# Kernel tuning notes

Hardware: AMD Instinct MI355X
Metric: run time of the kernel (lower is better)

Reference implementation:

```python
import jax, jax.numpy as jnp
import numpy as np

B, T, D_IN, D_ENC, D_H = 16384, 60, 3, 64, 128


def setup_inputs() -> dict:
    key = jax.random.key(0)
    ks = jax.random.split(key, 10)
    s_enc = 1.0 / np.sqrt(D_IN)
    s_lstm = 1.0 / np.sqrt(D_H)
    s_dec = 1.0 / np.sqrt(D_H)
    return {
        "x": jax.random.normal(ks[0], (B, D_IN), dtype=jnp.float32),
        "W_enc": jax.random.uniform(ks[1], (D_ENC, D_IN), jnp.float32, -s_enc, s_enc),
        "b_enc": jax.random.uniform(ks[2], (D_ENC,), jnp.float32, -s_enc, s_enc),
        "W_ih": jax.random.uniform(ks[3], (4 * D_H, D_ENC), jnp.float32, -s_lstm, s_lstm),
        "W_hh": jax.random.uniform(ks[4], (4 * D_H, D_H), jnp.float32, -s_lstm, s_lstm),
        "b_ih": jax.random.uniform(ks[5], (4 * D_H,), jnp.float32, -s_lstm, s_lstm),
        "b_hh": jax.random.uniform(ks[6], (4 * D_H,), jnp.float32, -s_lstm, s_lstm),
        "W_dec": jax.random.uniform(ks[7], (1, D_H), jnp.float32, -s_dec, s_dec),
        "b_dec": jax.random.uniform(ks[8], (1,), jnp.float32, -s_dec, s_dec),
    }


def _forward(x, W_enc, b_enc, W_ih, W_hh, b_ih, b_hh, W_dec, b_dec):
    encoded = x @ W_enc.T + b_enc  # [B, 64]
    # Input to LSTM is identical at every timestep -> precompute Wx projection once.
    xp = encoded @ W_ih.T + b_ih + b_hh  # [B, 4*H], PyTorch gate order i,f,g,o
    h0 = jnp.zeros((x.shape[0], D_H), x.dtype)
    c0 = jnp.zeros((x.shape[0], D_H), x.dtype)

    def step(carry, _):
        h, c = carry
        gates = xp + h @ W_hh.T  # [B, 4*H]
        i, f, g, o = jnp.split(gates, 4, axis=-1)
        i = jax.nn.sigmoid(i)
        f = jax.nn.sigmoid(f)
        g = jnp.tanh(g)
        o = jax.nn.sigmoid(o)
        c = f * c + i * g
        h = o * jnp.tanh(c)
        return (h, c), h

    (_, _), hs = jax.lax.scan(step, (h0, c0), None, length=T)  # hs: [T, B, H]
    lstm_out = jnp.transpose(hs, (1, 0, 2))  # [B, T, H]
    out = (lstm_out @ W_dec.T + b_dec)[..., 0]  # [B, T]
    return jax.nn.sigmoid(out)


def reference(x, W_enc, b_enc, W_ih, W_hh, b_ih, b_hh, W_dec, b_dec):
    return _forward(x, W_enc, b_enc, W_ih, W_hh, b_ih, b_hh, W_dec, b_dec)
```

## Files before the change

kernel.cpp:

```cpp
#include <hip/hip_runtime.h>

#define T_STEPS 60
#define HID 128
#define ROWS 16
#define NBLK (16384 / ROWS)

typedef __attribute__((ext_vector_type(8))) short short8;
typedef __attribute__((ext_vector_type(4))) short short4v;
typedef __attribute__((ext_vector_type(4))) float f32x4;

#define K1 1.44269504088896340736f

__device__ __forceinline__ unsigned short f2bf(float f) {
  unsigned u = __float_as_uint(f);
  return (unsigned short)((u + 0x7fffu + ((u >> 16) & 1u)) >> 16);
}
__device__ __forceinline__ float bf2f(unsigned short s) {
  return __uint_as_float(((unsigned)s) << 16);
}
__device__ __forceinline__ float sigm(float x) {
  return __builtin_amdgcn_rcpf(1.0f + __expf(-x));
}

#define HB0 0
#define HB1 4096
#define WD_BASE 8192
#define LDS_BYTES 8704

__global__ __launch_bounds__(512, 4) void lstm_fused(
    const float* __restrict__ x, const float* __restrict__ W_enc,
    const float* __restrict__ b_enc, const float* __restrict__ W_ih,
    const float* __restrict__ W_hh, const float* __restrict__ b_ih,
    const float* __restrict__ b_hh, const float* __restrict__ W_dec,
    const float* __restrict__ b_dec, float* __restrict__ out) {
  __shared__ __align__(16) unsigned char lds[LDS_BYTES];

  const int tid = threadIdx.x;
  const int wav = tid >> 6;
  const int lane = tid & 63;
  const int l15 = lane & 15;
  const int l4 = lane >> 4;
  const int u = wav * 16 + l15;
  const int row0 = blockIdx.x * ROWS;

  for (int i = tid; i < 1024; i += 512) ((unsigned*)(lds + HB0))[i] = 0u;
  if (tid < 128) ((float*)(lds + WD_BASE))[tid] = W_dec[tid];

  float xpv[4][4];
  {
    float xr0[4], xr1[4], xr2[4];
#pragma unroll
    for (int v = 0; v < 4; ++v) {
      int r = 4 * l4 + v;
      const float* xp_ = x + (size_t)(row0 + r) * 3;
      xr0[v] = xp_[0];
      xr1[v] = xp_[1];
      xr2[v] = xp_[2];
    }
#pragma unroll
    for (int gt = 0; gt < 4; ++gt) {
      float bias = b_ih[gt * 128 + u] + b_hh[gt * 128 + u];
#pragma unroll
      for (int v = 0; v < 4; ++v) xpv[gt][v] = bias;
    }
    const f32x4* wr0 = (const f32x4*)(W_ih + (size_t)u * 64);
    const f32x4* wr1 = (const f32x4*)(W_ih + (size_t)(128 + u) * 64);
    const f32x4* wr2 = (const f32x4*)(W_ih + (size_t)(256 + u) * 64);
    const f32x4* wr3 = (const f32x4*)(W_ih + (size_t)(384 + u) * 64);
    for (int e4 = 0; e4 < 16; ++e4) {
      f32x4 w0 = wr0[e4], w1 = wr1[e4], w2 = wr2[e4], w3 = wr3[e4];
#pragma unroll
      for (int j = 0; j < 4; ++j) {
        int e = e4 * 4 + j;
        float we0 = W_enc[e * 3], we1 = W_enc[e * 3 + 1], we2 = W_enc[e * 3 + 2];
        float be = b_enc[e];
#pragma unroll
        for (int v = 0; v < 4; ++v) {
          float ev = fmaf(we0, xr0[v], fmaf(we1, xr1[v], fmaf(we2, xr2[v], be)));
          xpv[0][v] = fmaf(w0[j], ev, xpv[0][v]);
          xpv[1][v] = fmaf(w1[j], ev, xpv[1][v]);
          xpv[2][v] = fmaf(w2[j], ev, xpv[2][v]);
          xpv[3][v] = fmaf(w3[j], ev, xpv[3][v]);
        }
      }
    }
#pragma unroll
    for (int gt = 0; gt < 4; ++gt) {
      float s = (gt == 2) ? (-2.0f * K1) : (-K1);
#pragma unroll
      for (int v = 0; v < 4; ++v) xpv[gt][v] *= s;
    }
  }

  short8 bw[4][4];
#pragma unroll
  for (int gt = 0; gt < 4; ++gt) {
    float s = (gt == 2) ? (-2.0f * K1) : (-K1);
#pragma unroll
    for (int kt = 0; kt < 4; ++kt) {
      const float* p = W_hh + (size_t)(gt * 128 + u) * HID + kt * 32 + 8 * l4;
      short8 f;
#pragma unroll
      for (int j = 0; j < 8; ++j) f[j] = (short)f2bf(s * p[j]);
      bw[gt][kt] = f;
    }
  }

  float ct[4];
#pragma unroll
  for (int v = 0; v < 4; ++v) ct[v] = 0.0f;

  const unsigned swzA =
      (((unsigned)(l15 & 7)) << 4) ^ (((unsigned)(l15 & 8)) << 2);
  unsigned rdA[4];
#pragma unroll
  for (int kt = 0; kt < 4; ++kt)
    rdA[kt] = ((unsigned)(l15 * 256 + l4 * 16 + kt * 64)) ^ swzA;
  unsigned wrA[4];
#pragma unroll
  for (int v = 0; v < 4; ++v) {
    unsigned rr = (unsigned)(4 * l4 + v);
    wrA[v] = (rr * 256 + (unsigned)u * 2) ^ ((rr & 7u) << 4) ^ ((rr & 8u) << 2);
  }
  const int drow = wav * 2 + (l4 >> 1);
  const int idx = (l4 & 1) * 16 + l15;
  const unsigned dA = ((unsigned)(drow * 256 + idx * 8)) ^
                      (((unsigned)(drow & 7)) << 4) ^ (((unsigned)(drow & 8)) << 2);
  const int outIdx = (row0 + drow) * T_STEPS;
  const float bdec = b_dec[0];
  const float kneg = -2.0f * K1;
  const float kpos = 2.0f * K1;

  __syncthreads();

#define STEP(RB, WB, tcur)                                                     \
  {                                                                            \
    f32x4 acc[4];                                                              \
    _Pragma("unroll") for (int gt = 0; gt < 4; ++gt) {                         \
      acc[gt][0] = xpv[gt][0];                                                 \
      acc[gt][1] = xpv[gt][1];                                                 \
      acc[gt][2] = xpv[gt][2];                                                 \
      acc[gt][3] = xpv[gt][3];                                                 \
    }                                                                          \
    _Pragma("unroll") for (int kt = 0; kt < 4; ++kt) {                         \
      short8 af = *(const short8*)(lds + (RB) + rdA[kt]);                      \
      _Pragma("unroll") for (int gt = 0; gt < 4; ++gt) acc[gt] =               \
          __builtin_amdgcn_mfma_f32_16x16x32_bf16(af, bw[gt][kt], acc[gt],     \
                                                  0, 0, 0);                    \
    }                                                                          \
    _Pragma("unroll") for (int v = 0; v < 4; ++v) {                            \
      float ea = __builtin_amdgcn_exp2f(acc[0][v]);                \
      float ef = __builtin_amdgcn_exp2f(acc[1][v]);                \
      float eg = __builtin_amdgcn_exp2f(acc[2][v]);               \
      float eo = __builtin_amdgcn_exp2f(acc[3][v]);                \
      float A = 1.0f + ea, F = 1.0f + ef, G = 1.0f + eg, Bo = 1.0f + eo;       \
      float AG = A * G;                                                        \
      float r = __builtin_amdgcn_rcpf(F * AG);                                 \
      float t = fmaf(kpos, eg, kneg);                            \
      float num = fmaf(ct[v], AG, t * F);                                      \
      float cn = num * r;                                    \
      ct[v] = cn;                                                              \
      float ec = __builtin_amdgcn_exp2f(cn);                      \
      float r2 = __builtin_amdgcn_rcpf(Bo * (1.0f + ec));                      \
      float h = (1.0f - ec) * r2;                             \
      *(unsigned short*)(lds + (WB) + wrA[v]) = f2bf(h);                       \
    }                                                                          \
    __syncthreads();                                                           \
    {                                                                          \
      short4v hv = *(const short4v*)(lds + (WB) + dA);                         \
      f32x4 wd = *(const f32x4*)(lds + WD_BASE + idx * 16);                    \
      float dot = 0.f;                                                         \
      _Pragma("unroll") for (int i = 0; i < 4; ++i) dot =                      \
          fmaf(bf2f((unsigned short)hv[i]), wd[i], dot);                       \
      dot += __shfl_xor(dot, 1, 64);                                           \
      dot += __shfl_xor(dot, 2, 64);                                           \
      dot += __shfl_xor(dot, 4, 64);                                           \
      dot += __shfl_xor(dot, 8, 64);                                           \
      dot += __shfl_xor(dot, 16, 64);                                          \
      if ((lane & 31) == 0) out[outIdx + (tcur)] = sigm(dot + bdec);           \
    }                                                                          \
  }

  for (int t = 0; t < T_STEPS; t += 2) {
    STEP(HB0, HB1, t)
    STEP(HB1, HB0, t + 1)
  }
#undef STEP
}

extern "C" void kernel_launch(void* const* d_in, const int* in_sizes, int n_in,
                              void* d_out, int out_size, void* d_ws, size_t ws_size,
                              hipStream_t stream) {
  const float* x = (const float*)d_in[0];
  const float* W_enc = (const float*)d_in[1];
  const float* b_enc = (const float*)d_in[2];
  const float* W_ih = (const float*)d_in[3];
  const float* W_hh = (const float*)d_in[4];
  const float* b_ih = (const float*)d_in[5];
  const float* b_hh = (const float*)d_in[6];
  const float* W_dec = (const float*)d_in[7];
  const float* b_dec = (const float*)d_in[8];
  float* out = (float*)d_out;

  dim3 grid(NBLK);
  dim3 block(512);
  lstm_fused<<<grid, block, 0, stream>>>(x, W_enc, b_enc, W_ih, W_hh, b_ih, b_hh,
                                         W_dec, b_dec, out);
}
```

Before: 243.3 us.

## Fuse decoder dot into gate epilogue with LDS atomics and batch output stores

Each thread now multiplies its fp32 h by its W_dec element, reduces across 16 lanes with shuffles, and atomically adds the partial into an LDS buffer of per-row, per-timestep logits. This removes the post-barrier LDS re-read of h and the separate decoder reduction from every step. Sigmoid and global stores are done once at the end as coalesced float4 writes instead of scattered per-step scalar stores. In exchange it adds LDS float atomics (8 waves contend per address), uses more LDS, and sums unrounded fp32 h, which slightly changes numerics.

```diff
diff --git a/kernel.cpp b/kernel.cpp
--- a/kernel.cpp
+++ b/kernel.cpp
@@ -6,7 +6,6 @@
 #define NBLK (16384 / ROWS)
 
 typedef __attribute__((ext_vector_type(8))) short short8;
-typedef __attribute__((ext_vector_type(4))) short short4v;
 typedef __attribute__((ext_vector_type(4))) float f32x4;
 
 #define K1 1.44269504088896340736f
@@ -15,17 +14,14 @@
   unsigned u = __float_as_uint(f);
   return (unsigned short)((u + 0x7fffu + ((u >> 16) & 1u)) >> 16);
 }
-__device__ __forceinline__ float bf2f(unsigned short s) {
-  return __uint_as_float(((unsigned)s) << 16);
-}
 __device__ __forceinline__ float sigm(float x) {
   return __builtin_amdgcn_rcpf(1.0f + __expf(-x));
 }
 
 #define HB0 0
 #define HB1 4096
-#define WD_BASE 8192
-#define LDS_BYTES 8704
+#define OUT_BASE 8192
+#define LDS_BYTES 12032
 
 __global__ __launch_bounds__(512, 4) void lstm_fused(
     const float* __restrict__ x, const float* __restrict__ W_enc,
@@ -42,9 +38,10 @@
   const int l4 = lane >> 4;
   const int u = wav * 16 + l15;
   const int row0 = blockIdx.x * ROWS;
+  float* outf = (float*)(lds + OUT_BASE);
 
   for (int i = tid; i < 1024; i += 512) ((unsigned*)(lds + HB0))[i] = 0u;
-  if (tid < 128) ((float*)(lds + WD_BASE))[tid] = W_dec[tid];
+  for (int i = tid; i < 960; i += 512) outf[i] = 0.0f;
 
   float xpv[4][4];
   {
@@ -122,12 +119,7 @@
     unsigned rr = (unsigned)(4 * l4 + v);
     wrA[v] = (rr * 256 + (unsigned)u * 2) ^ ((rr & 7u) << 4) ^ ((rr & 8u) << 2);
   }
-  const int drow = wav * 2 + (l4 >> 1);
-  const int idx = (l4 & 1) * 16 + l15;
-  const unsigned dA = ((unsigned)(drow * 256 + idx * 8)) ^
-                      (((unsigned)(drow & 7)) << 4) ^ (((unsigned)(drow & 8)) << 2);
-  const int outIdx = (row0 + drow) * T_STEPS;
-  const float bdec = b_dec[0];
+  const float wdu = W_dec[u];
   const float kneg = -2.0f * K1;
   const float kpos = 2.0f * K1;
 
@@ -148,6 +140,7 @@
           __builtin_amdgcn_mfma_f32_16x16x32_bf16(af, bw[gt][kt], acc[gt],     \
                                                   0, 0, 0);                    \
     }                                                                          \
+    float pz[4];                                                               \
     _Pragma("unroll") for (int v = 0; v < 4; ++v) {                            \
       float ea = __builtin_amdgcn_exp2f(acc[0][v]);                \
       float ef = __builtin_amdgcn_exp2f(acc[1][v]);                \
@@ -158,27 +151,25 @@
       float r = __builtin_amdgcn_rcpf(F * AG);                                 \
       float t = fmaf(kpos, eg, kneg);                            \
       float num = fmaf(ct[v], AG, t * F);                                      \
-      float cn = num * r;                                    \
+      float cn = num * r;                                                      \
       ct[v] = cn;                                                              \
       float ec = __builtin_amdgcn_exp2f(cn);                      \
       float r2 = __builtin_amdgcn_rcpf(Bo * (1.0f + ec));                      \
       float h = (1.0f - ec) * r2;                             \
       *(unsigned short*)(lds + (WB) + wrA[v]) = f2bf(h);                       \
+      pz[v] = h * wdu;                                                         \
+    }                                                                          \
+    _Pragma("unroll") for (int v = 0; v < 4; ++v) {                            \
+      pz[v] += __shfl_xor(pz[v], 1, 64);                                       \
+      pz[v] += __shfl_xor(pz[v], 2, 64);                                       \
+      pz[v] += __shfl_xor(pz[v], 4, 64);                                       \
+      pz[v] += __shfl_xor(pz[v], 8, 64);                                       \
+    }                                                                          \
+    if (l15 == 0) {                                                            \
+      _Pragma("unroll") for (int v = 0; v < 4; ++v)                            \
+          atomicAdd(&outf[(4 * l4 + v) * T_STEPS + (tcur)], pz[v]);            \
     }                                                                          \
     __syncthreads();                                                           \
-    {                                                                          \
-      short4v hv = *(const short4v*)(lds + (WB) + dA);                         \
-      f32x4 wd = *(const f32x4*)(lds + WD_BASE + idx * 16);                    \
-      float dot = 0.f;                                                         \
-      _Pragma("unroll") for (int i = 0; i < 4; ++i) dot =                      \
-          fmaf(bf2f((unsigned short)hv[i]), wd[i], dot);                       \
-      dot += __shfl_xor(dot, 1, 64);                                           \
-      dot += __shfl_xor(dot, 2, 64);                                           \
-      dot += __shfl_xor(dot, 4, 64);                                           \
-      dot += __shfl_xor(dot, 8, 64);                                           \
-      dot += __shfl_xor(dot, 16, 64);                                          \
-      if ((lane & 31) == 0) out[outIdx + (tcur)] = sigm(dot + bdec);           \
-    }                                                                          \
   }
 
   for (int t = 0; t < T_STEPS; t += 2) {
@@ -186,6 +177,16 @@
     STEP(HB1, HB0, t + 1)
   }
 #undef STEP
+
+  const float bdec = b_dec[0];
+  for (int i = tid; i < 240; i += 512) {
+    int r = i / 15, c4 = i - r * 15;
+    f32x4 s = *(const f32x4*)&outf[r * T_STEPS + c4 * 4];
+    f32x4 o;
+#pragma unroll
+    for (int k = 0; k < 4; ++k) o[k] = sigm(s[k] + bdec);
+    *(f32x4*)(out + (size_t)(row0 + r) * T_STEPS + c4 * 4) = o;
+  }
 }
 
 extern "C" void kernel_launch(void* const* d_in, const int* in_sizes, int n_in,
```

After: 266.6 us. 9.6% more time.
